# Kernel tuning notes

Hardware: AMD Instinct MI355X
Metric: run time of the kernel (lower is better)

The kernel has to match this reference:

```python
import jax, jax.numpy as jnp
import numpy as np

K = 4096
N = 11008
GROUP_SIZE = 128
KG = K // GROUP_SIZE  # 32


def setup_inputs() -> dict:
    key = jax.random.key(0)
    k1, k2, k3 = jax.random.split(key, 3)
    x = jax.random.normal(k1, (4, 4096, K), dtype=jnp.float16)
    # packed INT4 weights: two 4-bit values per byte (stored as int32 in [0,256))
    weight_packed = jax.random.randint(k2, (N, K // 2), 0, 256, dtype=jnp.int32)
    # per-group scales, positive, ~0.1 scale like torch.randn().abs()*0.1
    scales = (jnp.abs(jax.random.normal(k3, (N, KG), dtype=jnp.float32)) * 0.1).astype(jnp.float16)
    return {"x": x, "weight_packed": weight_packed, "scales": scales}


def _dequant(weight_packed, scales):
    # low nibble -> even k, high nibble -> odd k
    low = (weight_packed & 0x0F).astype(jnp.float16)   # (N, K/2)
    high = ((weight_packed >> 4) & 0x0F).astype(jnp.float16)
    q = jnp.stack([low, high], axis=-1).reshape(N, K)  # interleave: k0=low, k1=high
    # broadcast scales over each group of GROUP_SIZE along K
    s = jnp.repeat(scales, GROUP_SIZE, axis=1)         # (N, K)
    return (q - jnp.float16(8.0)) * s                  # (N, K) fp16


def reference(x, weight_packed, scales):
    w = _dequant(weight_packed, scales)                # (N, K) fp16
    b, s_len, _ = x.shape
    x2d = x.reshape(-1, K)                             # (b*s, K)
    out2d = jnp.matmul(x2d, w.T)                       # (b*s, N) fp16 GEMM
    return out2d.reshape(b, s_len, N)
```

## Files before the change

### kernel.cpp

```cpp
#include <hip/hip_runtime.h>
#include <hip/hip_bf16.h>

#define KD 4096
#define ND 11008
#define MD 16384
#define KGD 32
#define NT (KD / 64)

typedef __hip_bfloat16 bf16;
typedef float f32x4 __attribute__((ext_vector_type(4)));
typedef short bf16x8 __attribute__((ext_vector_type(8)));

#define WAITV(n) asm volatile("s_waitcnt vmcnt(" #n ")" ::: "memory")

__device__ __forceinline__ void gload16(const bf16* g, bf16* l) {
    __builtin_amdgcn_global_load_lds((const __attribute__((address_space(1))) void*)g,
                                     (__attribute__((address_space(3))) void*)l, 16, 0, 0);
}

__global__ void cvt_kernel(const float* __restrict__ x, bf16* __restrict__ y, int n8) {
    int i = blockIdx.x * blockDim.x + threadIdx.x;
    if (i >= n8) return;
    const f32x4* p = reinterpret_cast<const f32x4*>(x + (size_t)i * 8);
    f32x4 a = p[0], b = p[1];
    bf16 o[8];
#pragma unroll
    for (int e = 0; e < 4; ++e) {
        o[e]     = __float2bfloat16(a[e]);
        o[4 + e] = __float2bfloat16(b[e]);
    }
    *reinterpret_cast<bf16x8*>(y + (size_t)i * 8) = *reinterpret_cast<bf16x8*>(o);
}

__global__ void dequant_kernel(const int* __restrict__ wp, const float* __restrict__ sc,
                               bf16* __restrict__ wd, int n0, int rows) {
    const int per_row = KD / 8;
    int t = blockIdx.x * blockDim.x + threadIdx.x;
    if (t >= rows * per_row) return;
    int lr = t / per_row;
    int q  = t - lr * per_row;
    int n  = n0 + lr;
    int j  = q * 4;
    const int4 p = *reinterpret_cast<const int4*>(wp + (size_t)n * (KD / 2) + j);
    float s = sc[(size_t)n * KGD + (j >> 6)];
    int v[4] = {p.x, p.y, p.z, p.w};
    bf16 o[8];
#pragma unroll
    for (int i = 0; i < 4; ++i) {
        o[2 * i]     = __float2bfloat16((float)((v[i] & 0xF) - 8) * s);
        o[2 * i + 1] = __float2bfloat16((float)(((v[i] >> 4) & 0xF) - 8) * s);
    }
    *reinterpret_cast<bf16x8*>(wd + (size_t)lr * KD + j * 2) = *reinterpret_cast<bf16x8*>(o);
}

__global__ __launch_bounds__(512, 2) void gemm256(const bf16* __restrict__ A,
                                                  const bf16* __restrict__ B,
                                                  float* __restrict__ C,
                                                  int mtiles, int ntiles, int n0base) {
    __shared__ bf16 lds[2][2][2][8192];
    const int tid  = threadIdx.x;
    const int lane = tid & 63;
    const int w    = tid >> 6;

    int nwg = mtiles * ntiles;
    int orig = blockIdx.x;
    int q8 = nwg >> 3, r8 = nwg & 7;
    int xcd = orig & 7, off = orig >> 3;
    int wg = (xcd < r8 ? xcd * (q8 + 1) : r8 * (q8 + 1) + (xcd - r8) * q8) + off;
    const int mb = wg / ntiles, nb = wg - mb * ntiles;
    const int m0 = mb * 256, n0 = nb * 256;

    const int wm = w >> 2, wn = w & 3;
    const int rl = lane & 15, kq = lane >> 4;
    const int sz = (rl >> 1) & 3;
    const int ro = 8 * (kq ^ sz);

    const int src_c = (((lane & 3) ^ ((lane >> 3) & 3)) << 3);
    const int src_r = (w << 4) + (lane >> 2);
    const bf16* Abase = A + (size_t)(m0 + src_r) * KD + src_c;
    const bf16* Bbase = B + (size_t)(n0 + src_r) * KD + src_c;

    f32x4 acc[8][4] = {};

    auto stage = [&](int buf, int kh, int k0) {
        const bf16* ga = Abase + k0 + kh * 32;
        const bf16* gb = Bbase + k0 + kh * 32;
        bf16* la = &lds[buf][kh][0][w * 512];
        bf16* lb = &lds[buf][kh][1][w * 512];
        gload16(ga, la);
        gload16(ga + (size_t)128 * KD, la + 4096);
        gload16(gb, lb);
        gload16(gb + (size_t)128 * KD, lb + 4096);
    };

    auto compute = [&](int buf, int kh) {
        const bf16* ua = &lds[buf][kh][0][0];
        const bf16* ub = &lds[buf][kh][1][0];
        bf16x8 af[8], bfr[4];
#pragma unroll
        for (int mi = 0; mi < 8; ++mi)
            af[mi] = *reinterpret_cast<const bf16x8*>(&ua[(wm * 128 + mi * 16 + rl) * 32 + ro]);
#pragma unroll
        for (int ni = 0; ni < 4; ++ni)
            bfr[ni] = *reinterpret_cast<const bf16x8*>(&ub[(wn * 64 + ni * 16 + rl) * 32 + ro]);
        __builtin_amdgcn_s_setprio(1);
#pragma unroll
        for (int mi = 0; mi < 8; ++mi)
#pragma unroll
            for (int ni = 0; ni < 4; ++ni)
                acc[mi][ni] = __builtin_amdgcn_mfma_f32_16x16x32_bf16(
                    af[mi], bfr[ni], acc[mi][ni], 0, 0, 0);
        __builtin_amdgcn_s_setprio(0);
    };

    stage(0, 0, 0);
    stage(0, 1, 0);

    for (int t = 0; t < NT - 1; ++t) {
        const int cur = t & 1, nxt = cur ^ 1, k0n = (t + 1) * 64;
        stage(nxt, 0, k0n);
        stage(nxt, 1, k0n);
        WAITV(8);
        __builtin_amdgcn_s_barrier();
        compute(cur, 0);
        compute(cur, 1);
    }
    WAITV(0);
    __builtin_amdgcn_s_barrier();
    compute(1, 0);
    compute(1, 1);

    const int crow = m0 + wm * 128 + kq * 4;
    const int ccol = n0base + n0 + wn * 64 + rl;
#pragma unroll
    for (int mi = 0; mi < 8; ++mi) {
#pragma unroll
        for (int r = 0; r < 4; ++r) {
            float* cp = C + (size_t)(crow + mi * 16 + r) * ND + ccol;
#pragma unroll
            for (int ni = 0; ni < 4; ++ni)
                cp[ni * 16] = acc[mi][ni][r];
        }
    }
}

extern "C" void kernel_launch(void* const* d_in, const int* in_sizes, int n_in,
                              void* d_out, int out_size, void* d_ws, size_t ws_size,
                              hipStream_t stream) {
    const float* x  = (const float*)d_in[0];
    const int*   wp = (const int*)d_in[1];
    const float* sc = (const float*)d_in[2];
    float* out = (float*)d_out;

    long long rows_cap = (long long)(ws_size / ((size_t)KD * 2));
    int mc, nc;
    if (rows_cap >= MD + 256) {
        mc = MD;
        long long r = rows_cap - MD;
        nc = (int)((r / 256) * 256);
        if (nc > ND) nc = ND;
    } else if (rows_cap >= ND + 256) {
        nc = ND;
        long long r = rows_cap - ND;
        mc = (int)((r / 256) * 256);
        if (mc > MD) mc = MD;
    } else {
        nc = (int)(((rows_cap / 2) / 256) * 256);
        if (nc > ND) nc = ND;
        long long r = rows_cap - nc;
        mc = (int)((r / 256) * 256);
        if (mc > MD) mc = MD;
        if (mc <= 0 || nc <= 0) return;
    }

    bf16* xbuf = (bf16*)d_ws;
    bf16* wbuf = xbuf + (size_t)mc * KD;

    for (int m0 = 0; m0 < MD; m0 += mc) {
        int mrows = (MD - m0 < mc) ? (MD - m0) : mc;
        int n8 = mrows * (KD / 8);
        cvt_kernel<<<(n8 + 255) / 256, 256, 0, stream>>>(x + (size_t)m0 * KD, xbuf, n8);
        for (int n0 = 0; n0 < ND; n0 += nc) {
            int nrows = (ND - n0 < nc) ? (ND - n0) : nc;
            int tt = nrows * (KD / 8);
            dequant_kernel<<<(tt + 255) / 256, 256, 0, stream>>>(wp, sc, wbuf, n0, nrows);
            int mt = mrows / 256, nt2 = nrows / 256;
            gemm256<<<mt * nt2, 512, 0, stream>>>(xbuf, wbuf, out + (size_t)m0 * ND, mt, nt2, n0);
        }
    }
}
```

Baseline: 1.414 ms.

## Restructure GEMM main loop into fine-grained interleaved load/MFMA phases

Replaces the simple double-buffered loop with an eight-phase-per-iteration schedule. Each phase reads half the A fragments from LDS, issues one global-to-LDS stage for A or B, synchronizes, then runs 16 MFMAs. Individual half-tiles are refilled as soon as they are consumed, which spreads memory traffic and overlaps it more finely with compute. The cost is more barriers per K step and fragile hand-tuned vmcnt accounting that must match the number of outstanding loads exactly.

```diff
diff --git a/kernel.cpp b/kernel.cpp
--- a/kernel.cpp
+++ b/kernel.cpp
@@ -12,6 +12,8 @@
 typedef short bf16x8 __attribute__((ext_vector_type(8)));
 
 #define WAITV(n) asm volatile("s_waitcnt vmcnt(" #n ")" ::: "memory")
+#define BAR()    asm volatile("s_barrier" ::: "memory")
+#define LGKM0()  asm volatile("s_waitcnt lgkmcnt(0)" ::: "memory")
 
 __device__ __forceinline__ void gload16(const bf16* g, bf16* l) {
     __builtin_amdgcn_global_load_lds((const __attribute__((address_space(1))) void*)g,
@@ -81,54 +83,84 @@
     const bf16* Bbase = B + (size_t)(n0 + src_r) * KD + src_c;
 
     f32x4 acc[8][4] = {};
-
-    auto stage = [&](int buf, int kh, int k0) {
-        const bf16* ga = Abase + k0 + kh * 32;
-        const bf16* gb = Bbase + k0 + kh * 32;
-        bf16* la = &lds[buf][kh][0][w * 512];
-        bf16* lb = &lds[buf][kh][1][w * 512];
+    bf16x8 afr[4], bfr[4];
+
+    auto stA = [&](int b, int k, int k0) {
+        const bf16* ga = Abase + k0 + k * 32;
+        bf16* la = &lds[b][k][0][w * 512];
         gload16(ga, la);
         gload16(ga + (size_t)128 * KD, la + 4096);
+    };
+    auto stB = [&](int b, int k, int k0) {
+        const bf16* gb = Bbase + k0 + k * 32;
+        bf16* lb = &lds[b][k][1][w * 512];
         gload16(gb, lb);
         gload16(gb + (size_t)128 * KD, lb + 4096);
     };
 
-    auto compute = [&](int buf, int kh) {
-        const bf16* ua = &lds[buf][kh][0][0];
-        const bf16* ub = &lds[buf][kh][1][0];
-        bf16x8 af[8], bfr[4];
-#pragma unroll
-        for (int mi = 0; mi < 8; ++mi)
-            af[mi] = *reinterpret_cast<const bf16x8*>(&ua[(wm * 128 + mi * 16 + rl) * 32 + ro]);
-#pragma unroll
-        for (int ni = 0; ni < 4; ++ni)
-            bfr[ni] = *reinterpret_cast<const bf16x8*>(&ub[(wn * 64 + ni * 16 + rl) * 32 + ro]);
-        __builtin_amdgcn_s_setprio(1);
-#pragma unroll
-        for (int mi = 0; mi < 8; ++mi)
-#pragma unroll
-            for (int ni = 0; ni < 4; ++ni)
-                acc[mi][ni] = __builtin_amdgcn_mfma_f32_16x16x32_bf16(
-                    af[mi], bfr[ni], acc[mi][ni], 0, 0, 0);
-        __builtin_amdgcn_s_setprio(0);
-    };
-
-    stage(0, 0, 0);
-    stage(0, 1, 0);
-
-    for (int t = 0; t < NT - 1; ++t) {
-        const int cur = t & 1, nxt = cur ^ 1, k0n = (t + 1) * 64;
-        stage(nxt, 0, k0n);
-        stage(nxt, 1, k0n);
-        WAITV(8);
-        __builtin_amdgcn_s_barrier();
-        compute(cur, 0);
-        compute(cur, 1);
-    }
-    WAITV(0);
-    __builtin_amdgcn_s_barrier();
-    compute(1, 0);
-    compute(1, 1);
+#define PHASE_A(bufi, khi, STAGE, VM) do {                                          \
+    const bf16* ua_ = &lds[bufi][khi][0][0];                                        \
+    const bf16* ub_ = &lds[bufi][khi][1][0];                                        \
+    _Pragma("unroll") for (int m_ = 0; m_ < 4; ++m_)                                \
+        afr[m_] = *reinterpret_cast<const bf16x8*>(                                 \
+            &ua_[(wm * 128 + m_ * 16 + rl) * 32 + ro]);                             \
+    _Pragma("unroll") for (int n_ = 0; n_ < 4; ++n_)                                \
+        bfr[n_] = *reinterpret_cast<const bf16x8*>(                                 \
+            &ub_[(wn * 64 + n_ * 16 + rl) * 32 + ro]);                              \
+    STAGE;                                                                          \
+    BAR(); LGKM0();                                                                 \
+    __builtin_amdgcn_s_setprio(1);                                                  \
+    _Pragma("unroll") for (int m_ = 0; m_ < 4; ++m_)                                \
+        _Pragma("unroll") for (int n_ = 0; n_ < 4; ++n_)                            \
+            acc[m_][n_] = __builtin_amdgcn_mfma_f32_16x16x32_bf16(                  \
+                afr[m_], bfr[n_], acc[m_][n_], 0, 0, 0);                            \
+    __builtin_amdgcn_s_setprio(0);                                                  \
+    VM; BAR();                                                                      \
+} while (0)
+
+#define PHASE_B(bufi, khi, STAGE, VM) do {                                          \
+    const bf16* ua_ = &lds[bufi][khi][0][0];                                        \
+    _Pragma("unroll") for (int m_ = 0; m_ < 4; ++m_)                                \
+        afr[m_] = *reinterpret_cast<const bf16x8*>(                                 \
+            &ua_[(wm * 128 + (4 + m_) * 16 + rl) * 32 + ro]);                       \
+    STAGE;                                                                          \
+    BAR(); LGKM0();                                                                 \
+    __builtin_amdgcn_s_setprio(1);                                                  \
+    _Pragma("unroll") for (int m_ = 0; m_ < 4; ++m_)                                \
+        _Pragma("unroll") for (int n_ = 0; n_ < 4; ++n_)                            \
+            acc[4 + m_][n_] = __builtin_amdgcn_mfma_f32_16x16x32_bf16(              \
+                afr[m_], bfr[n_], acc[4 + m_][n_], 0, 0, 0);                        \
+    __builtin_amdgcn_s_setprio(0);                                                  \
+    VM; BAR();                                                                      \
+} while (0)
+
+    stB(0, 0, 0); stA(0, 0, 0); stB(0, 1, 0); stA(0, 1, 0);
+    stB(1, 0, 64); stA(1, 0, 64); stB(1, 1, 64);
+    WAITV(6);
+    BAR();
+
+    for (int j = 0; j < NT / 2 - 1; ++j) {
+        const int t1 = (2 * j + 1) * 64, t2 = (2 * j + 2) * 64, t3 = (2 * j + 3) * 64;
+        PHASE_A(0, 0, stA(1, 1, t1), (void)0);
+        PHASE_B(0, 0, stB(0, 0, t2), (void)0);
+        PHASE_A(0, 1, stA(0, 0, t2), (void)0);
+        PHASE_B(0, 1, stB(0, 1, t2), WAITV(6));
+        PHASE_A(1, 0, stA(0, 1, t2), (void)0);
+        PHASE_B(1, 0, stB(1, 0, t3), (void)0);
+        PHASE_A(1, 1, stA(1, 0, t3), (void)0);
+        PHASE_B(1, 1, stB(1, 1, t3), WAITV(6));
+    }
+    PHASE_A(0, 0, stA(1, 1, (NT - 1) * 64), (void)0);
+    PHASE_B(0, 0, (void)0, (void)0);
+    PHASE_A(0, 1, (void)0, (void)0);
+    PHASE_B(0, 1, (void)0, WAITV(6));
+    PHASE_A(1, 0, (void)0, WAITV(4));
+    PHASE_B(1, 0, (void)0, WAITV(2));
+    PHASE_A(1, 1, (void)0, WAITV(0));
+    PHASE_B(1, 1, (void)0, (void)0);
+
+#undef PHASE_A
+#undef PHASE_B
 
     const int crow = m0 + wm * 128 + kq * 4;
     const int ccol = n0base + n0 + wn * 64 + rl;
```

After: 1.448 ms. +2.4%, slower.

## Switch GEMM to 4-wave blocks with 32x32x16 MFMA and 128x128 warp tiles

Applied to the files above, without the earlier changes.

The 256x256 GEMM tile is now computed by 4 waves instead of 8. Each wave owns a 128x128 sub-tile and accumulates with 32x32x16 bf16 MFMAs instead of 16x16x32. LDS fragment loads are interleaved with MFMA issue, and the pipeline adds a barrier before each stage. The aim is to cut LDS traffic per FLOP and raise MFMA efficiency. The cost is 256 accumulator registers per lane, one block per CU with fewer waves to hide latency, and a scattered output store pattern.

```diff
diff --git a/kernel.cpp b/kernel.cpp
--- a/kernel.cpp
+++ b/kernel.cpp
@@ -9,9 +9,11 @@
 
 typedef __hip_bfloat16 bf16;
 typedef float f32x4 __attribute__((ext_vector_type(4)));
+typedef float f32x16 __attribute__((ext_vector_type(16)));
 typedef short bf16x8 __attribute__((ext_vector_type(8)));
 
 #define WAITV(n) asm volatile("s_waitcnt vmcnt(" #n ")" ::: "memory")
+#define BAR()    asm volatile("s_barrier" ::: "memory")
 
 __device__ __forceinline__ void gload16(const bf16* g, bf16* l) {
     __builtin_amdgcn_global_load_lds((const __attribute__((address_space(1))) void*)g,
@@ -53,7 +55,7 @@
     *reinterpret_cast<bf16x8*>(wd + (size_t)lr * KD + j * 2) = *reinterpret_cast<bf16x8*>(o);
 }
 
-__global__ __launch_bounds__(512, 2) void gemm256(const bf16* __restrict__ A,
+__global__ __launch_bounds__(256, 1) void gemm256(const bf16* __restrict__ A,
                                                   const bf16* __restrict__ B,
                                                   float* __restrict__ C,
                                                   int mtiles, int ntiles, int n0base) {
@@ -70,76 +72,90 @@
     const int mb = wg / ntiles, nb = wg - mb * ntiles;
     const int m0 = mb * 256, n0 = nb * 256;
 
-    const int wm = w >> 2, wn = w & 3;
-    const int rl = lane & 15, kq = lane >> 4;
-    const int sz = (rl >> 1) & 3;
-    const int ro = 8 * (kq ^ sz);
-
-    const int src_c = (((lane & 3) ^ ((lane >> 3) & 3)) << 3);
-    const int src_r = (w << 4) + (lane >> 2);
-    const bf16* Abase = A + (size_t)(m0 + src_r) * KD + src_c;
-    const bf16* Bbase = B + (size_t)(n0 + src_r) * KD + src_c;
-
-    f32x4 acc[8][4] = {};
-
-    auto stage = [&](int buf, int kh, int k0) {
-        const bf16* ga = Abase + k0 + kh * 32;
-        const bf16* gb = Bbase + k0 + kh * 32;
-        bf16* la = &lds[buf][kh][0][w * 512];
-        bf16* lb = &lds[buf][kh][1][w * 512];
-        gload16(ga, la);
-        gload16(ga + (size_t)128 * KD, la + 4096);
-        gload16(gb, lb);
-        gload16(gb + (size_t)128 * KD, lb + 4096);
-    };
-
-    auto compute = [&](int buf, int kh) {
-        const bf16* ua = &lds[buf][kh][0][0];
-        const bf16* ub = &lds[buf][kh][1][0];
-        bf16x8 af[8], bfr[4];
-#pragma unroll
-        for (int mi = 0; mi < 8; ++mi)
-            af[mi] = *reinterpret_cast<const bf16x8*>(&ua[(wm * 128 + mi * 16 + rl) * 32 + ro]);
-#pragma unroll
-        for (int ni = 0; ni < 4; ++ni)
-            bfr[ni] = *reinterpret_cast<const bf16x8*>(&ub[(wn * 64 + ni * 16 + rl) * 32 + ro]);
-        __builtin_amdgcn_s_setprio(1);
-#pragma unroll
-        for (int mi = 0; mi < 8; ++mi)
-#pragma unroll
-            for (int ni = 0; ni < 4; ++ni)
-                acc[mi][ni] = __builtin_amdgcn_mfma_f32_16x16x32_bf16(
-                    af[mi], bfr[ni], acc[mi][ni], 0, 0, 0);
-        __builtin_amdgcn_s_setprio(0);
-    };
-
-    stage(0, 0, 0);
-    stage(0, 1, 0);
+    const int wm = w >> 1, wn = w & 1;
+    const int r5 = lane & 31, kc = lane >> 5;
+    const int q  = (r5 >> 1) & 3;
+    const int co0 = ((kc) ^ q) * 8;
+    const int co1 = ((2 + kc) ^ q) * 8;
+
+    const int srow = w * 64 + (lane >> 2);
+    const int scol = ((lane & 3) ^ ((lane >> 3) & 3)) * 8;
+    const bf16* Ab = A + (size_t)(m0 + srow) * KD + scol;
+    const bf16* Bb = B + (size_t)(n0 + srow) * KD + scol;
+
+    f32x16 acc[4][4] = {};
+
+    auto stage = [&](int b, int k0) {
+#pragma unroll
+        for (int kh = 0; kh < 2; ++kh) {
+            const bf16* ga = Ab + k0 + kh * 32;
+            const bf16* gb = Bb + k0 + kh * 32;
+#pragma unroll
+            for (int i = 0; i < 4; ++i) {
+                gload16(ga + (size_t)(i * 16) * KD, &lds[b][kh][0][(w * 64 + i * 16) * 32]);
+                gload16(gb + (size_t)(i * 16) * KD, &lds[b][kh][1][(w * 64 + i * 16) * 32]);
+            }
+        }
+    };
+
+    auto lA = [&](bf16x8* f, int b, int kh, int co) {
+#pragma unroll
+        for (int fm = 0; fm < 4; ++fm)
+            f[fm] = *reinterpret_cast<const bf16x8*>(
+                &lds[b][kh][0][(wm * 128 + fm * 32 + r5) * 32 + co]);
+    };
+    auto lB = [&](bf16x8* f, int b, int kh, int co) {
+#pragma unroll
+        for (int fn = 0; fn < 4; ++fn)
+            f[fn] = *reinterpret_cast<const bf16x8*>(
+                &lds[b][kh][1][(wn * 128 + fn * 32 + r5) * 32 + co]);
+    };
+    auto mm = [&](bf16x8* fa, bf16x8* fb) {
+#pragma unroll
+        for (int fm = 0; fm < 4; ++fm)
+#pragma unroll
+            for (int fn = 0; fn < 4; ++fn)
+                acc[fm][fn] = __builtin_amdgcn_mfma_f32_32x32x16_bf16(
+                    fa[fm], fb[fn], acc[fm][fn], 0, 0, 0);
+    };
+
+    auto compute = [&](int b) {
+        bf16x8 fa0[4], fb0[4], fa1[4], fb1[4];
+        lA(fa0, b, 0, co0); lB(fb0, b, 0, co0);
+        lA(fa1, b, 0, co1); lB(fb1, b, 0, co1);
+        mm(fa0, fb0);
+        lA(fa0, b, 1, co0); lB(fb0, b, 1, co0);
+        mm(fa1, fb1);
+        lA(fa1, b, 1, co1); lB(fb1, b, 1, co1);
+        mm(fa0, fb0);
+        mm(fa1, fb1);
+    };
+
+    stage(0, 0);
 
     for (int t = 0; t < NT - 1; ++t) {
-        const int cur = t & 1, nxt = cur ^ 1, k0n = (t + 1) * 64;
-        stage(nxt, 0, k0n);
-        stage(nxt, 1, k0n);
-        WAITV(8);
-        __builtin_amdgcn_s_barrier();
-        compute(cur, 0);
-        compute(cur, 1);
-    }
+        BAR();
+        stage((t + 1) & 1, (t + 1) * 64);
+        WAITV(16);
+        BAR();
+        compute(t & 1);
+    }
+    BAR();
     WAITV(0);
-    __builtin_amdgcn_s_barrier();
-    compute(1, 0);
-    compute(1, 1);
-
-    const int crow = m0 + wm * 128 + kq * 4;
-    const int ccol = n0base + n0 + wn * 64 + rl;
-#pragma unroll
-    for (int mi = 0; mi < 8; ++mi) {
-#pragma unroll
-        for (int r = 0; r < 4; ++r) {
-            float* cp = C + (size_t)(crow + mi * 16 + r) * ND + ccol;
-#pragma unroll
-            for (int ni = 0; ni < 4; ++ni)
-                cp[ni * 16] = acc[mi][ni][r];
+    BAR();
+    compute((NT - 1) & 1);
+
+    const int crow = m0 + wm * 128 + 4 * kc;
+    const int ccol = n0base + n0 + wn * 128 + r5;
+#pragma unroll
+    for (int fm = 0; fm < 4; ++fm) {
+#pragma unroll
+        for (int fn = 0; fn < 4; ++fn) {
+#pragma unroll
+            for (int r = 0; r < 16; ++r) {
+                int row = crow + fm * 32 + (r & 3) + 8 * (r >> 2);
+                C[(size_t)row * ND + ccol + fn * 32] = acc[fm][fn][r];
+            }
         }
     }
 }
@@ -185,7 +201,7 @@
             int tt = nrows * (KD / 8);
             dequant_kernel<<<(tt + 255) / 256, 256, 0, stream>>>(wp, sc, wbuf, n0, nrows);
             int mt = mrows / 256, nt2 = nrows / 256;
-            gemm256<<<mt * nt2, 512, 0, stream>>>(xbuf, wbuf, out + (size_t)m0 * ND, mt, nt2, n0);
+            gemm256<<<mt * nt2, 256, 0, stream>>>(xbuf, wbuf, out + (size_t)m0 * ND, mt, nt2, n0);
         }
     }
 }
```

New measurement: 1.837 ms. 29.9% more time.
